# Performance work log

Hardware: AMD Instinct MI355X
Metric: run time of the kernel (lower is better)

Reference implementation:

```python
import jax, jax.numpy as jnp
import numpy as np

K = 6

def _diag_indices(H, W):
    # stable argsort of anti-diagonal index i+j over row-major flattening
    i = np.arange(H)[:, None]
    j = np.arange(W)[None, :]
    order = np.argsort((i + j).ravel(), kind='stable')
    return order, np.argsort(order, kind='stable')

def _selective_scan(u, delta, A, Bs, Cs, D, delta_bias):
    # u, delta: (B,K,D,L); A: (K,D,N); Bs,Cs: (B,K,N,L); D,delta_bias: (K,D)
    delta = jax.nn.softplus(delta + delta_bias[None, :, :, None])
    dA = jnp.exp(jnp.einsum('bkdl,kdn->lbkdn', delta, A))          # (L,B,K,D,N)
    dBu = jnp.einsum('bkdl,bknl,bkdl->lbkdn', delta, Bs, u)         # (L,B,K,D,N)
    Cl = jnp.moveaxis(Cs, -1, 0)                                    # (L,B,K,N)
    x0 = jnp.zeros(dA.shape[1:], dA.dtype)
    def step(x, inp):
        dA_t, dBu_t, C_t = inp
        x = dA_t * x + dBu_t
        y = jnp.einsum('bkdn,bkn->bkd', x, C_t)
        return x, y
    _, ys = jax.lax.scan(step, x0, (dA, dBu, Cl))
    y = jnp.moveaxis(ys, 0, -1)                                     # (B,K,D,L)
    return y + u * D[None, :, :, None]

def reference(x, W_in, conv_w, conv_b, x_proj_w, dt_w, dt_b, A_logs, Ds, ln_g, ln_b, W_out):
    B, H, W, C = x.shape
    L = H * W
    di = dt_w.shape[1]
    dt_rank = dt_w.shape[2]
    N = A_logs.shape[1]
    # in_proj (no bias) and split
    xz = jnp.einsum('bhwc,oc->bhwo', x, W_in)
    xx, z = jnp.split(xz, 2, axis=-1)
    # depthwise conv 3x3, SAME padding, + bias, SiLU
    xc = jnp.transpose(xx, (0, 3, 1, 2))                            # (B,di,H,W)
    xc = jax.lax.conv_general_dilated(xc, conv_w, (1, 1), 'SAME',
            feature_group_count=di, dimension_numbers=('NCHW', 'OIHW', 'NCHW'))
    xc = jax.nn.silu(xc + conv_b[None, :, None, None])
    # build 6 scan orderings
    x_flat = xc.reshape(B, di, L)
    x_t = jnp.transpose(xc, (0, 1, 3, 2)).reshape(B, di, L)
    x_hwwh = jnp.stack([x_flat, x_t], axis=1)                       # (B,2,di,L)
    xs4 = jnp.concatenate([x_hwwh, x_hwwh[..., ::-1]], axis=1)      # (B,4,di,L)
    x_invhh = jnp.flip(xc, axis=-1).reshape(B, di, L)               # flip W only
    x_hh = jnp.stack([x_flat, x_invhh], axis=1)                     # (B,2,di,L)
    diag_idx, rev_idx = _diag_indices(H, W)
    xs = jnp.concatenate([xs4, x_hh[..., diag_idx]], axis=1)        # (B,6,di,L)
    # projections
    x_dbl = jnp.einsum('bkdl,kcd->bkcl', xs, x_proj_w)
    dts, Bs, Cs = jnp.split(x_dbl, [dt_rank, dt_rank + N], axis=2)
    dts = jnp.einsum('bkrl,kdr->bkdl', dts, dt_w)
    A = -jnp.exp(A_logs).reshape(K, di, N)
    out_y = _selective_scan(xs, dts, A, Bs, Cs, Ds.reshape(K, di), dt_b)
    # undo the 6 orderings
    inv_y = out_y[:, 2:4][..., ::-1]
    wh_y = jnp.transpose(out_y[:, 1].reshape(B, di, W, H), (0, 1, 3, 2)).reshape(B, di, L)
    invwh_y = jnp.transpose(inv_y[:, 1].reshape(B, di, W, H), (0, 1, 3, 2)).reshape(B, di, L)
    transhh = out_y[:, 4:6][..., rev_idx]
    invhh = transhh[:, 1][..., ::-1]
    y = out_y[:, 0] + inv_y[:, 0] + wh_y + invwh_y + transhh[:, 0] + invhh  # (B,di,L)
    y = jnp.transpose(y, (0, 2, 1)).reshape(B, H, W, di)
    # LayerNorm (eps=1e-5)
    mu = y.mean(-1, keepdims=True)
    var = ((y - mu) ** 2).mean(-1, keepdims=True)
    y = (y - mu) * jax.lax.rsqrt(var + 1e-5) * ln_g + ln_b
    y = y * jax.nn.silu(z)
    return jnp.einsum('bhwd,od->bhwo', y, W_out)

def setup_inputs():
    key = jax.random.key(0)
    ks = jax.random.split(key, 8)
    d_model, di, N, dt_rank = 64, 128, 16, 4
    x = jax.random.normal(ks[0], (1, 64, 64, d_model), jnp.float32)
    W_in = jax.random.normal(ks[1], (2 * di, d_model), jnp.float32) * d_model ** -0.5
    conv_w = jax.random.normal(ks[2], (di, 1, 3, 3), jnp.float32) / 3.0
    conv_b = jnp.zeros((di,), jnp.float32)
    x_proj_w = jax.random.normal(ks[3], (K, dt_rank + 2 * N, di), jnp.float32) * di ** -0.5
    s = dt_rank ** -0.5
    dt_w = jax.random.uniform(ks[4], (K, di, dt_rank), jnp.float32, -s, s)
    dt = jnp.exp(jax.random.uniform(ks[5], (K, di), jnp.float32)
                 * (np.log(0.1) - np.log(0.001)) + np.log(0.001))
    dt = jnp.clip(dt, 1e-4)
    dt_b = dt + jnp.log(-jnp.expm1(-dt))
    A_logs = jnp.log(jnp.tile(jnp.arange(1, N + 1, dtype=jnp.float32)[None, :], (K * di, 1)))
    Ds = jnp.ones((K * di,), jnp.float32)
    ln_g = jnp.ones((di,), jnp.float32)
    ln_b = jnp.zeros((di,), jnp.float32)
    W_out = jax.random.normal(ks[6], (d_model, di), jnp.float32) * di ** -0.5
    return {"x": x, "W_in": W_in, "conv_w": conv_w, "conv_b": conv_b,
            "x_proj_w": x_proj_w, "dt_w": dt_w, "dt_b": dt_b, "A_logs": A_logs,
            "Ds": Ds, "ln_g": ln_g, "ln_b": ln_b, "W_out": W_out}
```

## Files before the change

kernel.cpp:

```cpp
#include <hip/hip_runtime.h>
#include <math.h>

#define L    4096
#define DI   128
#define NS   16
#define KK   6
#define DTR  4
#define CM   64
#define NC   256
#define CH   (L/NC)

__device__ __forceinline__ float softplus_f(float x){
    return x > 20.f ? x : __logf(1.f + __expf(x));
}
__device__ __forceinline__ float silu_f(float x){
    return x / (1.f + __expf(-x));
}

__device__ __forceinline__ int rankp(int p){
    int h = p >> 6, w = p & 63, s = h + w;
    int imin = s > 63 ? s - 63 : 0;
    int off = (s < 64) ? (s*(s+1))/2 : 4096 - ((127-s)*(128-s))/2;
    return off + (h - imin);
}

__device__ __forceinline__ int perm_in(int k, int l, const int* __restrict__ diag){
    switch(k){
        case 0: return l;
        case 1: return ((l&63)<<6) | (l>>6);
        case 2: return (L-1) - l;
        case 3: { int m = (L-1)-l; return ((m&63)<<6) | (m>>6); }
        case 4: return diag[l];
        default: return diag[l] ^ 63;
    }
}

__global__ void k_diag(int* __restrict__ diag_idx){
    int p = blockIdx.x*256 + threadIdx.x;
    if(p >= L) return;
    diag_idx[rankp(p)] = p;
}

__global__ __launch_bounds__(256) void k_inproj(const float* __restrict__ x,
                                                const float* __restrict__ W_in,
                                                float* __restrict__ xx_t,
                                                float* __restrict__ sz){
    int pb = blockIdx.x * 16;
    int o  = threadIdx.x;
    __shared__ float xr[16][CM];
    ((float4*)&xr[0][0])[o] = ((const float4*)(x + (size_t)pb*CM))[o];
    float4 w[16];
    const float4* wrow = (const float4*)(W_in + (size_t)o*CM);
    #pragma unroll
    for(int q=0;q<16;q++) w[q] = wrow[q];
    __syncthreads();
    #pragma unroll
    for(int pi=0; pi<16; pi++){
        float acc = 0.f;
        const float4* xv4 = (const float4*)&xr[pi][0];
        #pragma unroll
        for(int q=0;q<16;q++){
            float4 xv = xv4[q];
            acc += w[q].x*xv.x + w[q].y*xv.y + w[q].z*xv.z + w[q].w*xv.w;
        }
        int p = pb + pi;
        if(o < DI) xx_t[(size_t)p*DI + o] = acc;
        else       sz[(size_t)p*DI + (o-DI)] = silu_f(acc);
    }
}

__global__ __launch_bounds__(256) void k_conv(const float* __restrict__ xx_t,
                                              const float* __restrict__ cw,
                                              const float* __restrict__ cb,
                                              float* __restrict__ xc_t){
    int idx = blockIdx.x*256 + threadIdx.x;
    int d = idx & 127, p = idx >> 7;
    int h = p >> 6, w = p & 63;
    float acc = cb[d];
    #pragma unroll
    for(int dh=-1; dh<=1; dh++){
        int hh = h+dh; if(hh < 0 || hh >= 64) continue;
        #pragma unroll
        for(int dw=-1; dw<=1; dw++){
            int ww = w+dw; if(ww < 0 || ww >= 64) continue;
            acc += cw[d*9 + (dh+1)*3+(dw+1)] * xx_t[(size_t)(hh*64+ww)*DI + d];
        }
    }
    xc_t[idx] = silu_f(acc);
}

#define XT_S 132
__global__ __launch_bounds__(256) void k_proj(const float* __restrict__ xc_t,
                                              const float* __restrict__ xpw,
                                              const int* __restrict__ diag,
                                              float* __restrict__ dts,
                                              float* __restrict__ BT,
                                              float* __restrict__ CT){
    int k  = blockIdx.x >> 6;
    int l0 = (blockIdx.x & 63) * 64;
    int t  = threadIdx.x;
    __shared__ float xt[64*XT_S];
    #pragma unroll
    for(int q=0;q<8;q++){
        int lin = q*256 + t;
        int row = lin >> 5, col4 = lin & 31;
        int p = perm_in(k, l0+row, diag);
        float4 v = ((const float4*)(xc_t + (size_t)p*DI))[col4];
        *((float4*)(xt + row*XT_S + col4*4)) = v;
    }
    __syncthreads();
    int l = t & 63, c0 = (t>>6)*9;
    const float* xr = xt + l*XT_S;
    float acc[9];
    #pragma unroll
    for(int j=0;j<9;j++) acc[j] = 0.f;
    const float4* wbase = (const float4*)(xpw + (size_t)k*36*DI);
    for(int dd4=0; dd4<32; dd4++){
        float4 xv = *((const float4*)(xr + dd4*4));
        #pragma unroll
        for(int j=0;j<9;j++){
            float4 wv = wbase[(c0+j)*32 + dd4];
            acc[j] += wv.x*xv.x + wv.y*xv.y + wv.z*xv.z + wv.w*xv.w;
        }
    }
    #pragma unroll
    for(int j=0;j<9;j++){
        int c = c0 + j;
        if(c < 4)        dts[((size_t)k*4 + c)*L + l0 + l] = acc[j];
        else if(c < 20)  BT[((size_t)k*L + l0 + l)*NS + (c-4)]  = acc[j];
        else             CT[((size_t)k*L + l0 + l)*NS + (c-20)] = acc[j];
    }
}

__global__ __launch_bounds__(128) void k_scan1(const float* __restrict__ xc_t,
                                               const float* __restrict__ dts,
                                               const float* __restrict__ BT,
                                               const float* __restrict__ dtw,
                                               const float* __restrict__ dtb,
                                               const float* __restrict__ A_logs,
                                               const int* __restrict__ diag,
                                               float* __restrict__ apb,
                                               float* __restrict__ xlb){
    int bk = blockIdx.x;
    int k = bk >> 8, cc = bk & (NC-1);
    int d = threadIdx.x;
    int l0 = cc*CH;

    __shared__ float Bt[CH*NS];
    __shared__ float dtt[4*CH];
    __shared__ int   pt[CH];

    if(d < 64) ((float4*)Bt)[d] = ((const float4*)(BT + ((size_t)k*L + l0)*NS))[d];
    else { int j = d-64; int r = j>>4, i = j&15;
           dtt[j] = dts[((size_t)k*4 + r)*L + l0 + i]; }
    if(d < CH) pt[d] = perm_in(k, l0+d, diag);
    __syncthreads();

    float4 w4 = ((const float4*)dtw)[(size_t)k*DI + d];
    float  bb = dtb[k*DI + d];
    float A[NS];
    {
        const float4* ar = (const float4*)(A_logs + ((size_t)k*DI + d)*NS);
        #pragma unroll
        for(int q=0;q<4;q++){
            float4 a4 = ar[q];
            A[q*4+0] = -__expf(a4.x); A[q*4+1] = -__expf(a4.y);
            A[q*4+2] = -__expf(a4.z); A[q*4+3] = -__expf(a4.w);
        }
    }
    float x[NS], ap[NS];
    #pragma unroll
    for(int n=0;n<NS;n++){ x[n] = 0.f; ap[n] = 1.f; }

    float u_nxt = xc_t[(size_t)pt[0]*DI + d];
    #pragma unroll
    for(int i=0;i<CH;i++){
        float u = u_nxt;
        if(i+1 < CH) u_nxt = xc_t[(size_t)pt[i+1]*DI + d];
        float dv = bb + w4.x*dtt[i] + w4.y*dtt[CH+i] + w4.z*dtt[2*CH+i] + w4.w*dtt[3*CH+i];
        float delta = softplus_f(dv);
        float du = delta*u;
        const float* Bi = Bt + i*NS;
        #pragma unroll
        for(int n=0;n<NS;n++){
            float da = __expf(delta*A[n]);
            x[n] = da*x[n] + du*Bi[n];
            ap[n] *= da;
        }
    }
    float* apd = apb + ((size_t)bk*DI + d)*NS;
    float* xld = xlb + ((size_t)bk*DI + d)*NS;
    #pragma unroll
    for(int q=0;q<4;q++){
        ((float4*)apd)[q] = make_float4(ap[q*4],ap[q*4+1],ap[q*4+2],ap[q*4+3]);
        ((float4*)xld)[q] = make_float4(x[q*4], x[q*4+1], x[q*4+2], x[q*4+3]);
    }
}

__global__ __launch_bounds__(256) void k_comb(float* __restrict__ apb,
                                              const float* __restrict__ xlb){
    int tid = blockIdx.x*256 + threadIdx.x;
    int k = tid >> 11, rem = tid & 2047;
    size_t base = (size_t)k*NC*2048 + rem;
    float run = 0.f;
    float a[8], xl[8];
    #pragma unroll
    for(int q=0;q<8;q++){ a[q] = apb[base + (size_t)q*2048]; xl[q] = xlb[base + (size_t)q*2048]; }
    for(int b=0; b<NC/8; b++){
        float a2[8], x2[8];
        if(b+1 < NC/8){
            #pragma unroll
            for(int q=0;q<8;q++){
                size_t off = base + (size_t)((b+1)*8+q)*2048;
                a2[q] = apb[off]; x2[q] = xlb[off];
            }
        }
        #pragma unroll
        for(int q=0;q<8;q++){
            size_t off = base + (size_t)(b*8+q)*2048;
            apb[off] = run;
            run = a[q]*run + xl[q];
        }
        #pragma unroll
        for(int q=0;q<8;q++){ a[q] = a2[q]; xl[q] = x2[q]; }
    }
}

__global__ __launch_bounds__(128) void k_scan2(const float* __restrict__ xc_t,
                                               const float* __restrict__ dts,
                                               const float* __restrict__ BT,
                                               const float* __restrict__ CT,
                                               const float* __restrict__ dtw,
                                               const float* __restrict__ dtb,
                                               const float* __restrict__ A_logs,
                                               const float* __restrict__ Dsv,
                                               const int* __restrict__ diag,
                                               const float* __restrict__ inib,
                                               float* __restrict__ yk){
    int bk = blockIdx.x;
    int k = bk >> 8, cc = bk & (NC-1);
    int d = threadIdx.x;
    int l0 = cc*CH;

    __shared__ float Bt[CH*NS];
    __shared__ float Ct[CH*NS];
    __shared__ float dtt[4*CH];
    __shared__ int   pt[CH];

    if(d < 64){
        ((float4*)Bt)[d] = ((const float4*)(BT + ((size_t)k*L + l0)*NS))[d];
        int r = d>>4, i = d&15;
        dtt[d] = dts[((size_t)k*4 + r)*L + l0 + i];
    } else {
        ((float4*)Ct)[d-64] = ((const float4*)(CT + ((size_t)k*L + l0)*NS))[d-64];
    }
    if(d < CH) pt[d] = perm_in(k, l0+d, diag);
    __syncthreads();

    float4 w4 = ((const float4*)dtw)[(size_t)k*DI + d];
    float  bb = dtb[k*DI + d];
    float  Dv = Dsv[k*DI + d];
    float A[NS];
    {
        const float4* ar = (const float4*)(A_logs + ((size_t)k*DI + d)*NS);
        #pragma unroll
        for(int q=0;q<4;q++){
            float4 a4 = ar[q];
            A[q*4+0] = -__expf(a4.x); A[q*4+1] = -__expf(a4.y);
            A[q*4+2] = -__expf(a4.z); A[q*4+3] = -__expf(a4.w);
        }
    }
    float x[NS];
    {
        const float4* ir = (const float4*)(inib + ((size_t)bk*DI + d)*NS);
        #pragma unroll
        for(int q=0;q<4;q++){
            float4 v = ir[q];
            x[q*4+0]=v.x; x[q*4+1]=v.y; x[q*4+2]=v.z; x[q*4+3]=v.w;
        }
    }

    float u_nxt = xc_t[(size_t)pt[0]*DI + d];
    #pragma unroll
    for(int i=0;i<CH;i++){
        float u = u_nxt;
        if(i+1 < CH) u_nxt = xc_t[(size_t)pt[i+1]*DI + d];
        float dv = bb + w4.x*dtt[i] + w4.y*dtt[CH+i] + w4.z*dtt[2*CH+i] + w4.w*dtt[3*CH+i];
        float delta = softplus_f(dv);
        float du = delta*u;
        const float* Bi = Bt + i*NS;
        const float* Ci = Ct + i*NS;
        float y = 0.f;
        #pragma unroll
        for(int n=0;n<NS;n++){
            float da = __expf(delta*A[n]);
            x[n] = da*x[n] + du*Bi[n];
            y += x[n]*Ci[n];
        }
        yk[((size_t)k*L + l0 + i)*DI + d] = y + u*Dv;
    }
}

__global__ __launch_bounds__(128) void k_out(const float* __restrict__ yk,
                                             const float* __restrict__ sz,
                                             const float* __restrict__ ln_g,
                                             const float* __restrict__ ln_b,
                                             const float* __restrict__ W_out,
                                             float* __restrict__ out){
    int pb = blockIdx.x*8;
    int d = threadIdx.x;
    __shared__ float ms[8][DI];
    __shared__ float red[8][2][2];
    float g = ln_g[d], bc = ln_b[d];
    float yv[8];
    #pragma unroll
    for(int pi=0;pi<8;pi++){
        int p = pb+pi;
        int tp = ((p&63)<<6) | (p>>6);
        float y;
        y  = yk[((size_t)0*L + p)*DI + d];
        y += yk[((size_t)1*L + tp)*DI + d];
        y += yk[((size_t)2*L + (L-1-p))*DI + d];
        y += yk[((size_t)3*L + (L-1-tp))*DI + d];
        y += yk[((size_t)4*L + rankp(p))*DI + d];
        y += yk[((size_t)5*L + rankp(L-1-p))*DI + d];
        yv[pi] = y;
        float s1 = y, s2 = y*y;
        #pragma unroll
        for(int m=1;m<64;m<<=1){ s1 += __shfl_xor(s1,m,64); s2 += __shfl_xor(s2,m,64); }
        if((d&63)==0){ red[pi][d>>6][0] = s1; red[pi][d>>6][1] = s2; }
    }
    __syncthreads();
    #pragma unroll
    for(int pi=0;pi<8;pi++){
        float mu  = (red[pi][0][0]+red[pi][1][0]) * (1.f/DI);
        float var = (red[pi][0][1]+red[pi][1][1]) * (1.f/DI) - mu*mu;
        float yh = (yv[pi]-mu)*rsqrtf(var+1e-5f)*g + bc;
        ms[pi][d] = yh * sz[(size_t)(pb+pi)*DI + d];
    }
    __syncthreads();
    int o = d & 63, hf = d >> 6;
    float4 w[32];
    const float4* wr4 = (const float4*)(W_out + (size_t)o*DI);
    #pragma unroll
    for(int q=0;q<32;q++) w[q] = wr4[q];
    for(int pi=hf; pi<8; pi+=2){
        float acc = 0.f;
        const float4* mr = (const float4*)ms[pi];
        #pragma unroll
        for(int q=0;q<32;q++){
            float4 xv = mr[q];
            acc += w[q].x*xv.x + w[q].y*xv.y + w[q].z*xv.z + w[q].w*xv.w;
        }
        out[(size_t)(pb+pi)*CM + o] = acc;
    }
}

extern "C" void kernel_launch(void* const* d_in, const int* in_sizes, int n_in,
                              void* d_out, int out_size, void* d_ws, size_t ws_size,
                              hipStream_t stream) {
    const float* x      = (const float*)d_in[0];
    const float* W_in   = (const float*)d_in[1];
    const float* conv_w = (const float*)d_in[2];
    const float* conv_b = (const float*)d_in[3];
    const float* xpw    = (const float*)d_in[4];
    const float* dtw    = (const float*)d_in[5];
    const float* dtb    = (const float*)d_in[6];
    const float* A_logs = (const float*)d_in[7];
    const float* Dsv    = (const float*)d_in[8];
    const float* ln_g   = (const float*)d_in[9];
    const float* ln_b   = (const float*)d_in[10];
    const float* W_out  = (const float*)d_in[11];
    float* out = (float*)d_out;

    float* ws = (float*)d_ws;
    float* xx_t = ws;
    float* sz   = xx_t + (size_t)L*DI;
    float* xc_t = sz   + (size_t)L*DI;
    float* dts  = xc_t + (size_t)L*DI;
    float* BT   = dts  + (size_t)KK*4*L;
    float* CT   = BT   + (size_t)KK*L*NS;
    float* apb  = CT   + (size_t)KK*L*NS;
    float* xlb  = apb  + (size_t)KK*NC*DI*NS;
    float* yk   = xlb  + (size_t)KK*NC*DI*NS;
    int*   diag = (int*)(yk + (size_t)KK*L*DI);

    k_diag  <<<L/256, 256, 0, stream>>>(diag);
    k_inproj<<<L/16, 256, 0, stream>>>(x, W_in, xx_t, sz);
    k_conv  <<<(L*DI)/256, 256, 0, stream>>>(xx_t, conv_w, conv_b, xc_t);
    k_proj  <<<KK*64, 256, 0, stream>>>(xc_t, xpw, diag, dts, BT, CT);
    k_scan1 <<<KK*NC, 128, 0, stream>>>(xc_t, dts, BT, dtw, dtb, A_logs, diag, apb, xlb);
    k_comb  <<<KK*DI*NS/256, 256, 0, stream>>>(apb, xlb);
    k_scan2 <<<KK*NC, 128, 0, stream>>>(xc_t, dts, BT, CT, dtw, dtb, A_logs, Dsv, diag, apb, yk);
    k_out   <<<L/8, 128, 0, stream>>>(yk, sz, ln_g, ln_b, W_out, out);
}
```

Measured before the change: 195.5 us.

## Parallelize chunk-carry combine and coalesce projection weights via pre-transposed layout

```diff
diff --git a/kernel.cpp b/kernel.cpp
--- a/kernel.cpp
+++ b/kernel.cpp
@@ -35,37 +35,54 @@
     }
 }
 
-__global__ void k_diag(int* __restrict__ diag_idx){
-    int p = blockIdx.x*256 + threadIdx.x;
-    if(p >= L) return;
-    diag_idx[rankp(p)] = p;
+__global__ __launch_bounds__(256) void k_init(const float* __restrict__ W_in,
+                                              const float* __restrict__ W_out,
+                                              int* __restrict__ diag_idx,
+                                              float* __restrict__ WI4,
+                                              float* __restrict__ WO4){
+    int t = blockIdx.x*256 + threadIdx.x;
+    diag_idx[rankp(t)] = t;
+    {
+        int d4 = t >> 8, o = t & 255;
+        float4 v = make_float4(W_in[(size_t)o*CM + d4*4+0], W_in[(size_t)o*CM + d4*4+1],
+                               W_in[(size_t)o*CM + d4*4+2], W_in[(size_t)o*CM + d4*4+3]);
+        ((float4*)WI4)[d4*256 + o] = v;
+    }
+    if(t < 2048){
+        int d4 = t >> 6, o = t & 63;
+        float4 v = make_float4(W_out[(size_t)o*DI + d4*4+0], W_out[(size_t)o*DI + d4*4+1],
+                               W_out[(size_t)o*DI + d4*4+2], W_out[(size_t)o*DI + d4*4+3]);
+        ((float4*)WO4)[d4*64 + o] = v;
+    }
 }
 
 __global__ __launch_bounds__(256) void k_inproj(const float* __restrict__ x,
-                                                const float* __restrict__ W_in,
+                                                const float* __restrict__ WI4,
                                                 float* __restrict__ xx_t,
                                                 float* __restrict__ sz){
     int pb = blockIdx.x * 16;
     int o  = threadIdx.x;
     __shared__ float xr[16][CM];
     ((float4*)&xr[0][0])[o] = ((const float4*)(x + (size_t)pb*CM))[o];
-    float4 w[16];
-    const float4* wrow = (const float4*)(W_in + (size_t)o*CM);
-    #pragma unroll
-    for(int q=0;q<16;q++) w[q] = wrow[q];
-    __syncthreads();
-    #pragma unroll
-    for(int pi=0; pi<16; pi++){
-        float acc = 0.f;
-        const float4* xv4 = (const float4*)&xr[pi][0];
-        #pragma unroll
-        for(int q=0;q<16;q++){
-            float4 xv = xv4[q];
-            acc += w[q].x*xv.x + w[q].y*xv.y + w[q].z*xv.z + w[q].w*xv.w;
-        }
+    __syncthreads();
+    float acc[16];
+    #pragma unroll
+    for(int pi=0;pi<16;pi++) acc[pi] = 0.f;
+    const float4* W4 = (const float4*)WI4;
+    #pragma unroll
+    for(int d4=0; d4<16; d4++){
+        float4 wv = W4[d4*256 + o];
+        #pragma unroll
+        for(int pi=0; pi<16; pi++){
+            float4 xv = *((const float4*)&xr[pi][d4*4]);
+            acc[pi] += wv.x*xv.x + wv.y*xv.y + wv.z*xv.z + wv.w*xv.w;
+        }
+    }
+    #pragma unroll
+    for(int pi=0;pi<16;pi++){
         int p = pb + pi;
-        if(o < DI) xx_t[(size_t)p*DI + o] = acc;
-        else       sz[(size_t)p*DI + (o-DI)] = silu_f(acc);
+        if(o < DI) xx_t[(size_t)p*DI + o] = acc[pi];
+        else       sz[(size_t)p*DI + (o-DI)] = silu_f(acc[pi]);
     }
 }
 
@@ -197,32 +214,41 @@
     }
 }
 
-__global__ __launch_bounds__(256) void k_comb(float* __restrict__ apb,
+__global__ __launch_bounds__(512) void k_comb(float* __restrict__ apb,
                                               const float* __restrict__ xlb){
-    int tid = blockIdx.x*256 + threadIdx.x;
-    int k = tid >> 11, rem = tid & 2047;
-    size_t base = (size_t)k*NC*2048 + rem;
-    float run = 0.f;
-    float a[8], xl[8];
-    #pragma unroll
-    for(int q=0;q<8;q++){ a[q] = apb[base + (size_t)q*2048]; xl[q] = xlb[base + (size_t)q*2048]; }
-    for(int b=0; b<NC/8; b++){
-        float a2[8], x2[8];
-        if(b+1 < NC/8){
-            #pragma unroll
-            for(int q=0;q<8;q++){
-                size_t off = base + (size_t)((b+1)*8+q)*2048;
-                a2[q] = apb[off]; x2[q] = xlb[off];
-            }
-        }
-        #pragma unroll
-        for(int q=0;q<8;q++){
-            size_t off = base + (size_t)(b*8+q)*2048;
-            apb[off] = run;
-            run = a[q]*run + xl[q];
-        }
-        #pragma unroll
-        for(int q=0;q<8;q++){ a[q] = a2[q]; xl[q] = x2[q]; }
+    int k    = blockIdx.x >> 5;
+    int gidx = blockIdx.x & 31;
+    int seg  = threadIdx.x >> 6;
+    int c    = threadIdx.x & 63;
+    int rem  = gidx*64 + c;
+    size_t sb = (size_t)k*NC*2048 + (size_t)seg*32*2048 + rem;
+    float a[32], xl[32];
+    #pragma unroll
+    for(int j=0;j<32;j++){
+        a[j]  = apb[sb + (size_t)j*2048];
+        xl[j] = xlb[sb + (size_t)j*2048];
+    }
+    float Aag = 1.f, Xag = 0.f;
+    #pragma unroll
+    for(int j=0;j<32;j++){ Xag = a[j]*Xag + xl[j]; Aag *= a[j]; }
+    __shared__ float sA[64][8], sX[64][8];
+    sA[c][seg] = Aag; sX[c][seg] = Xag;
+    __syncthreads();
+    if(threadIdx.x < 64){
+        float run = 0.f;
+        #pragma unroll
+        for(int s=0;s<8;s++){
+            float at = sA[c][s], xt = sX[c][s];
+            sX[c][s] = run;
+            run = at*run + xt;
+        }
+    }
+    __syncthreads();
+    float run = sX[c][seg];
+    #pragma unroll
+    for(int j=0;j<32;j++){
+        apb[sb + (size_t)j*2048] = run;
+        run = a[j]*run + xl[j];
     }
 }
 
@@ -305,7 +331,7 @@
                                              const float* __restrict__ sz,
                                              const float* __restrict__ ln_g,
                                              const float* __restrict__ ln_b,
-                                             const float* __restrict__ W_out,
+                                             const float* __restrict__ WO4,
                                              float* __restrict__ out){
     int pb = blockIdx.x*8;
     int d = threadIdx.x;
@@ -339,21 +365,23 @@
         ms[pi][d] = yh * sz[(size_t)(pb+pi)*DI + d];
     }
     __syncthreads();
-    int o = d & 63, hf = d >> 6;
-    float4 w[32];
-    const float4* wr4 = (const float4*)(W_out + (size_t)o*DI);
-    #pragma unroll
-    for(int q=0;q<32;q++) w[q] = wr4[q];
-    for(int pi=hf; pi<8; pi+=2){
-        float acc = 0.f;
-        const float4* mr = (const float4*)ms[pi];
-        #pragma unroll
-        for(int q=0;q<32;q++){
-            float4 xv = mr[q];
-            acc += w[q].x*xv.x + w[q].y*xv.y + w[q].z*xv.z + w[q].w*xv.w;
-        }
-        out[(size_t)(pb+pi)*CM + o] = acc;
-    }
+    int o = d & 63, w = d >> 6;
+    const float4* W4 = (const float4*)WO4;
+    float acc[4];
+    #pragma unroll
+    for(int q=0;q<4;q++) acc[q] = 0.f;
+    #pragma unroll
+    for(int d4=0; d4<32; d4++){
+        float4 wv = W4[d4*64 + o];
+        #pragma unroll
+        for(int q=0;q<4;q++){
+            float4 xv = *((const float4*)&ms[w*4+q][d4*4]);
+            acc[q] += wv.x*xv.x + wv.y*xv.y + wv.z*xv.z + wv.w*xv.w;
+        }
+    }
+    #pragma unroll
+    for(int q=0;q<4;q++)
+        out[(size_t)(pb + w*4 + q)*CM + o] = acc[q];
 }
 
 extern "C" void kernel_launch(void* const* d_in, const int* in_sizes, int n_in,
@@ -384,13 +412,15 @@
     float* xlb  = apb  + (size_t)KK*NC*DI*NS;
     float* yk   = xlb  + (size_t)KK*NC*DI*NS;
     int*   diag = (int*)(yk + (size_t)KK*L*DI);
-
-    k_diag  <<<L/256, 256, 0, stream>>>(diag);
-    k_inproj<<<L/16, 256, 0, stream>>>(x, W_in, xx_t, sz);
+    float* WI4  = (float*)(diag + L);
+    float* WO4  = WI4 + (size_t)16*256*4;
+
+    k_init  <<<L/256, 256, 0, stream>>>(W_in, W_out, diag, WI4, WO4);
+    k_inproj<<<L/16, 256, 0, stream>>>(x, WI4, xx_t, sz);
     k_conv  <<<(L*DI)/256, 256, 0, stream>>>(xx_t, conv_w, conv_b, xc_t);
     k_proj  <<<KK*64, 256, 0, stream>>>(xc_t, xpw, diag, dts, BT, CT);
     k_scan1 <<<KK*NC, 128, 0, stream>>>(xc_t, dts, BT, dtw, dtb, A_logs, diag, apb, xlb);
-    k_comb  <<<KK*DI*NS/256, 256, 0, stream>>>(apb, xlb);
+    k_comb  <<<KK*32, 512, 0, stream>>>(apb, xlb);
     k_scan2 <<<KK*NC, 128, 0, stream>>>(xc_t, dts, BT, CT, dtw, dtb, A_logs, Dsv, diag, apb, yk);
-    k_out   <<<L/8, 128, 0, stream>>>(yk, sz, ln_g, ln_b, W_out, out);
-}
+    k_out   <<<L/8, 128, 0, stream>>>(yk, sz, ln_g, ln_b, WO4, out);
+}
```

Result: slower. 228.4 us (+16.8%).
